# Kernel tuning notes

Measured on AMD Instinct MI355X. Metric: run time of the kernel, lower is better.

## Reference

```python
import math
import jax, jax.numpy as jnp
import numpy as np

B, S, H = 4, 2048, 1024

def setup_inputs() -> dict:
    key = jax.random.key(0)
    k1, k2, k3, k4 = jax.random.split(key, 4)
    X = jax.random.normal(k1, (B, S, H), dtype=jnp.float32)
    attention_mask = jax.random.randint(k2, (B, S), 0, 2).astype(jnp.bool_)
    W = jax.random.normal(k3, (H, 3 * H), dtype=jnp.float32) * (1.0 / math.sqrt(H))
    b = jax.random.normal(k4, (3 * H,), dtype=jnp.float32) * 0.02
    return {"X": X, "attention_mask": attention_mask, "W": W, "b": b}

def reference(X, attention_mask, W, b):
    hidden_dim = X.shape[-1]
    # fused QKV projection: (B,S,3H)
    QKV = X @ W + b
    Q, K, V = jnp.split(QKV, 3, axis=-1)
    # scores: (B, S, S)
    scores = jnp.einsum('bqd,bkd->bqk', Q, K) / math.sqrt(hidden_dim)
    # 2D key-padding mask (B,S) -> broadcast over query dim; True = masked
    mask = attention_mask[:, None, :]  # (B,1,S) broadcasts to (B,S,S)
    scores = jnp.where(mask, -jnp.inf, scores)
    attn = jax.nn.softmax(scores, axis=-1)
    # dropout_rate = 0.0 (eval): identity
    return jnp.einsum('bqk,bkd->bqd', attn, V)
```

## Files before the change

kernel.cpp:

```cpp
#include <hip/hip_runtime.h>
#include <hip/hip_bf16.h>
#include <stdint.h>


typedef __attribute__((ext_vector_type(8))) short bf16x8;
typedef __attribute__((ext_vector_type(4))) float f32x4;

__device__ __forceinline__ void async_cp16(const void* g, void* l) {
  __builtin_amdgcn_global_load_lds(
      (const __attribute__((address_space(1))) void*)g,
      (__attribute__((address_space(3))) void*)l, 16, 0, 0);
}

__global__ void cvt_f32_bf16(const float* __restrict__ s,
                             __hip_bfloat16* __restrict__ d, int n) {
  int i = (blockIdx.x * blockDim.x + threadIdx.x) * 4;
  if (i >= n) return;
  float4 f = *(const float4*)(s + i);
  __hip_bfloat16 o[4];
  o[0] = __float2bfloat16(f.x);
  o[1] = __float2bfloat16(f.y);
  o[2] = __float2bfloat16(f.z);
  o[3] = __float2bfloat16(f.w);
  *(ushort4*)(d + i) = *(const ushort4*)o;
}

__global__ void transpose_cvt_f32(const float* __restrict__ src, int srcld,
                                  __hip_bfloat16* __restrict__ dst, int dstld) {
  __shared__ float tile[32][33];
  int bx = blockIdx.x * 32;
  int by = blockIdx.y * 32;
  int tx = threadIdx.x, ty = threadIdx.y;
#pragma unroll
  for (int j = 0; j < 4; ++j)
    tile[ty + j * 8][tx] = src[(int64_t)(by + ty + j * 8) * srcld + bx + tx];
  __syncthreads();
#pragma unroll
  for (int j = 0; j < 4; ++j)
    dst[(int64_t)(bx + ty + j * 8) * dstld + by + tx] =
        __float2bfloat16(tile[tx][ty + j * 8]);
}

__global__ __launch_bounds__(256) void mask_scan(const int* __restrict__ mask,
                                                 int* __restrict__ idx,
                                                 int* __restrict__ cnt,
                                                 int* __restrict__ cnt_pad) {
  const int b = blockIdx.x;
  mask += b * 2048;
  idx += b * 2048;
  const int t = threadIdx.x;
  const int lane = t & 63, wave = t >> 6;

  int keep[8];
  int local = 0;
#pragma unroll
  for (int j = 0; j < 8; ++j) {
    keep[j] = (mask[t * 8 + j] == 0);
    local += keep[j];
  }
  int pre = local;
#pragma unroll
  for (int off = 1; off <= 32; off <<= 1) {
    int n = __shfl_up(pre, off, 64);
    if (lane >= off) pre += n;
  }
  __shared__ int wsum[4];
  if (lane == 63) wsum[wave] = pre;
  __syncthreads();
  int base = 0;
  for (int w = 0; w < wave; ++w) base += wsum[w];
  int excl = base + pre - local;
#pragma unroll
  for (int j = 0; j < 8; ++j)
    if (keep[j]) idx[excl++] = t * 8 + j;
  if (t == 255) {
    int tot = base + pre;
    cnt[b] = tot;
    cnt_pad[b] = (tot + 127) & ~127;
  }
}

__global__ __launch_bounds__(256) void gemm_qkv(
    const __hip_bfloat16* __restrict__ Xb, const __hip_bfloat16* __restrict__ Wt,
    const float* __restrict__ bias, const int* __restrict__ idx,
    const int* __restrict__ cnt, const int* __restrict__ cnt_pad,
    __hip_bfloat16* __restrict__ Q, __hip_bfloat16* __restrict__ Kc,
    __hip_bfloat16* __restrict__ Vt) {
  const int z = blockIdx.z;
  const int f = blockIdx.x;
  const int xcd = f & 7, loc = f >> 3;
  const int m0 = ((loc & 7) * 2 + (xcd >> 2)) * 128;
  const int n_idx = (loc >> 3) * 4 + (xcd & 3);
  const bool isQ = (n_idx < 8);
  if (!isQ && m0 >= cnt_pad[z]) return;
  const int n0 = (isQ ? n_idx : n_idx - 8) * 128;
  const __hip_bfloat16* A = Xb + (int64_t)z * 2048 * 1024;
  const __hip_bfloat16* Bt = Wt + (isQ ? 0 : (int64_t)1024 * 1024);
  const float* bv = bias + (isQ ? 0 : 1024);

  const int tid = threadIdx.x;
  const int wave = tid >> 6, lane = tid & 63;
  const int quad = lane >> 4, tr = lane & 15;
  const int wm = wave & 1, wn = wave >> 1;

  __shared__ __hip_bfloat16 ls[17408];
  __hip_bfloat16* lsA = ls;
  __hip_bfloat16* lsB = ls + 8192;

  const __hip_bfloat16* gsrc[8];
  __hip_bfloat16* ldst[8];
  {
    const int srow = lane >> 3;
    const int kc = (((lane & 7) ^ srow) * 8);
    const int cz = isQ ? 0 : cnt[z];
    const int* idxz = idx + z * 2048;
#pragma unroll
    for (int cc = 0; cc < 8; ++cc) {
      int c = wave * 8 + cc;
      int isA = (c < 16);
      int cr = isA ? c : (c - 16);
      int row = cr * 8 + srow;
      if (isA) {
        int ar = m0 + row;
        if (!isQ) ar = (ar < cz) ? idxz[ar] : 0;
        gsrc[cc] = A + (int64_t)ar * 1024 + kc;
      } else {
        gsrc[cc] = Bt + (int64_t)(n0 + row) * 1024 + kc;
      }
      ldst[cc] = (isA ? lsA : lsB) + cr * 512;
    }
  }

  f32x4 acc[4][4];
#pragma unroll
  for (int mi = 0; mi < 4; ++mi)
#pragma unroll
    for (int ni = 0; ni < 4; ++ni) acc[mi][ni] = (f32x4){0.f, 0.f, 0.f, 0.f};

  const int t7 = tr & 7;

  for (int k0 = 0; k0 < 1024; k0 += 64) {
    __syncthreads();
#pragma unroll
    for (int cc = 0; cc < 8; ++cc) async_cp16(gsrc[cc] + k0, ldst[cc]);
    __syncthreads();

#pragma unroll
    for (int w = 0; w < 2; ++w) {
      const int sl = ((w << 2) | quad) ^ t7;
      bf16x8 af[4], bfv[4];
#pragma unroll
      for (int mi = 0; mi < 4; ++mi)
        af[mi] = *(const bf16x8*)(lsA + (wm * 64 + mi * 16 + tr) * 64 + sl * 8);
#pragma unroll
      for (int ni = 0; ni < 4; ++ni)
        bfv[ni] = *(const bf16x8*)(lsB + (wn * 64 + ni * 16 + tr) * 64 + sl * 8);
#pragma unroll
      for (int mi = 0; mi < 4; ++mi)
#pragma unroll
        for (int ni = 0; ni < 4; ++ni)
          acc[mi][ni] = __builtin_amdgcn_mfma_f32_16x16x32_bf16(
              af[mi], bfv[ni], acc[mi][ni], 0, 0, 0);
    }
  }

  const int rowbase = m0 + wm * 64;
  const int colbase = n0 + wn * 64;
  if (isQ) {
    __hip_bfloat16* C = Q + (int64_t)z * 2048 * 1024;
#pragma unroll
    for (int ni = 0; ni < 4; ++ni) {
      int col = colbase + ni * 16 + tr;
      float bb = bv[col];
#pragma unroll
      for (int mi = 0; mi < 4; ++mi) {
        int row = rowbase + mi * 16 + quad * 4;
#pragma unroll
        for (int r = 0; r < 4; ++r)
          C[(int64_t)(row + r) * 1024 + col] =
              __float2bfloat16(acc[mi][ni][r] + bb);
      }
    }
  } else if (n0 < 1024) {
    __hip_bfloat16* C = Kc + (int64_t)z * 2048 * 1024;
#pragma unroll
    for (int ni = 0; ni < 4; ++ni) {
      int col = colbase + ni * 16 + tr;
      float bb = bv[col];
#pragma unroll
      for (int mi = 0; mi < 4; ++mi) {
        int row = rowbase + mi * 16 + quad * 4;
#pragma unroll
        for (int r = 0; r < 4; ++r)
          C[(int64_t)(row + r) * 1024 + col] =
              __float2bfloat16(acc[mi][ni][r] + bb);
      }
    }
  } else {
    __syncthreads();
#pragma unroll
    for (int ni = 0; ni < 4; ++ni) {
      int cl = wn * 64 + ni * 16 + tr;
      float bb = bv[colbase + ni * 16 + tr];
#pragma unroll
      for (int mi = 0; mi < 4; ++mi) {
        int rl = wm * 64 + mi * 16 + quad * 4;
        __hip_bfloat16 h[4];
#pragma unroll
        for (int r = 0; r < 4; ++r) h[r] = __float2bfloat16(acc[mi][ni][r] + bb);
        *(ushort4*)(ls + cl * 136 + rl) = *(const ushort4*)h;
      }
    }
    __syncthreads();
    __hip_bfloat16* Vz = Vt + (int64_t)z * 1024 * 2048;
    const int d0 = n0 - 1024;
    const int seg = tid & 15;
#pragma unroll
    for (int p = 0; p < 8; ++p) {
      int d = p * 16 + (tid >> 4);
      bf16x8 v = *(const bf16x8*)(ls + d * 136 + seg * 8);
      *(bf16x8*)(Vz + (int64_t)(d0 + d) * 2048 + m0 + seg * 8) = v;
    }
  }
}

__global__ __launch_bounds__(256) void gemm_scores(
    const __hip_bfloat16* __restrict__ Qb, const __hip_bfloat16* __restrict__ Kc,
    __hip_bfloat16* __restrict__ Sc, float* __restrict__ rowsum,
    const int* __restrict__ cnt, const int* __restrict__ cnt_pad,
    float scale2) {
  const int z = blockIdx.z;
  const int f = blockIdx.x;
  const int xcd = f & 7, loc = f >> 3;
  const int m0 = ((loc & 7) * 2 + (xcd >> 2)) * 128;
  const int n0 = ((loc >> 3) * 4 + (xcd & 3)) * 64;
  if (n0 >= cnt_pad[z]) return;
  const __hip_bfloat16* A = Qb + (int64_t)z * 2048 * 1024;
  const __hip_bfloat16* Bt = Kc + (int64_t)z * 2048 * 1024;

  const int tid = threadIdx.x;
  const int wave = tid >> 6, lane = tid & 63;
  const int quad = lane >> 4, tr = lane & 15;
  const int wm = wave & 1, wn = wave >> 1;

  __shared__ __hip_bfloat16 lsA[128 * 64];
  __shared__ __hip_bfloat16 lsB[64 * 64];

  const __hip_bfloat16* gsrc[6];
  __hip_bfloat16* ldst[6];
  {
    const int srow = lane >> 3;
    const int kc = (((lane & 7) ^ srow) * 8);
#pragma unroll
    for (int cc = 0; cc < 6; ++cc) {
      int c = wave * 6 + cc;
      int isA = (c < 16);
      int cr = isA ? c : (c - 16);
      int row = cr * 8 + srow;
      gsrc[cc] = isA ? (A + (int64_t)(m0 + row) * 1024 + kc)
                     : (Bt + (int64_t)(n0 + row) * 1024 + kc);
      ldst[cc] = (isA ? lsA : lsB) + cr * 512;
    }
  }

  f32x4 acc[4][2];
#pragma unroll
  for (int mi = 0; mi < 4; ++mi)
#pragma unroll
    for (int ni = 0; ni < 2; ++ni) acc[mi][ni] = (f32x4){0.f, 0.f, 0.f, 0.f};

  const int t7 = tr & 7;

  for (int k0 = 0; k0 < 1024; k0 += 64) {
    __syncthreads();
#pragma unroll
    for (int cc = 0; cc < 6; ++cc) async_cp16(gsrc[cc] + k0, ldst[cc]);
    __syncthreads();

#pragma unroll
    for (int w = 0; w < 2; ++w) {
      const int sl = ((w << 2) | quad) ^ t7;
      bf16x8 af[4], bfv[2];
#pragma unroll
      for (int mi = 0; mi < 4; ++mi)
        af[mi] = *(const bf16x8*)(lsA + (wm * 64 + mi * 16 + tr) * 64 + sl * 8);
#pragma unroll
      for (int ni = 0; ni < 2; ++ni)
        bfv[ni] = *(const bf16x8*)(lsB + (wn * 32 + ni * 16 + tr) * 64 + sl * 8);
#pragma unroll
      for (int mi = 0; mi < 4; ++mi)
#pragma unroll
        for (int ni = 0; ni < 2; ++ni)
          acc[mi][ni] = __builtin_amdgcn_mfma_f32_16x16x32_bf16(
              af[mi], bfv[ni], acc[mi][ni], 0, 0, 0);
    }
  }

  const int rowbase = m0 + wm * 64;
  const int colbase = n0 + wn * 32;
  const int cn = cnt[z];
  __hip_bfloat16* C = Sc + (int64_t)z * 2048 * 2048;

  float psum[4][4];
#pragma unroll
  for (int mi = 0; mi < 4; ++mi)
#pragma unroll
    for (int r = 0; r < 4; ++r) psum[mi][r] = 0.f;

#pragma unroll
  for (int ni = 0; ni < 2; ++ni) {
    int col = colbase + ni * 16 + tr;
    bool valid = (col < cn);
#pragma unroll
    for (int mi = 0; mi < 4; ++mi) {
      int row = rowbase + mi * 16 + quad * 4;
#pragma unroll
      for (int r = 0; r < 4; ++r) {
        float e = valid ? exp2f(acc[mi][ni][r] * scale2) : 0.f;
        C[(int64_t)(row + r) * 2048 + col] = __float2bfloat16(e);
        psum[mi][r] += e;
      }
    }
  }
#pragma unroll
  for (int off = 1; off <= 8; off <<= 1)
#pragma unroll
    for (int mi = 0; mi < 4; ++mi)
#pragma unroll
      for (int r = 0; r < 4; ++r)
        psum[mi][r] += __shfl_xor(psum[mi][r], off, 64);
  if (tr == 0) {
    float* rs = rowsum + z * 2048 + rowbase;
#pragma unroll
    for (int mi = 0; mi < 4; ++mi)
#pragma unroll
      for (int r = 0; r < 4; ++r)
        atomicAdd(&rs[mi * 16 + quad * 4 + r], psum[mi][r]);
  }
}

__global__ __launch_bounds__(256) void gemm_pv(
    const __hip_bfloat16* __restrict__ Sc, const __hip_bfloat16* __restrict__ Vt,
    float* __restrict__ out, const float* __restrict__ rowsum,
    const int* __restrict__ cnt_pad) {
  const int z = blockIdx.z;
  const int f = blockIdx.x;
  const int xcd = f & 7, loc = f >> 3;
  const int m0 = ((loc & 7) * 2 + (xcd >> 2)) * 128;
  const int n0 = ((loc >> 3) * 4 + (xcd & 3)) * 64;
  const int Ks = cnt_pad[z];
  const __hip_bfloat16* A = Sc + (int64_t)z * 2048 * 2048;
  const __hip_bfloat16* Bt = Vt + (int64_t)z * 1024 * 2048;

  const int tid = threadIdx.x;
  const int wave = tid >> 6, lane = tid & 63;
  const int quad = lane >> 4, tr = lane & 15;
  const int wm = wave & 1, wn = wave >> 1;

  __shared__ __hip_bfloat16 lsA[128 * 64];
  __shared__ __hip_bfloat16 lsB[64 * 64];

  const __hip_bfloat16* gsrc[6];
  __hip_bfloat16* ldst[6];
  {
    const int srow = lane >> 3;
    const int kc = (((lane & 7) ^ srow) * 8);
#pragma unroll
    for (int cc = 0; cc < 6; ++cc) {
      int c = wave * 6 + cc;
      int isA = (c < 16);
      int cr = isA ? c : (c - 16);
      int row = cr * 8 + srow;
      gsrc[cc] = isA ? (A + (int64_t)(m0 + row) * 2048 + kc)
                     : (Bt + (int64_t)(n0 + row) * 2048 + kc);
      ldst[cc] = (isA ? lsA : lsB) + cr * 512;
    }
  }

  f32x4 acc[4][2];
#pragma unroll
  for (int mi = 0; mi < 4; ++mi)
#pragma unroll
    for (int ni = 0; ni < 2; ++ni) acc[mi][ni] = (f32x4){0.f, 0.f, 0.f, 0.f};

  const int t7 = tr & 7;

  for (int k0 = 0; k0 < Ks; k0 += 64) {
    __syncthreads();
#pragma unroll
    for (int cc = 0; cc < 6; ++cc) async_cp16(gsrc[cc] + k0, ldst[cc]);
    __syncthreads();

#pragma unroll
    for (int w = 0; w < 2; ++w) {
      const int sl = ((w << 2) | quad) ^ t7;
      bf16x8 af[4], bfv[2];
#pragma unroll
      for (int mi = 0; mi < 4; ++mi)
        af[mi] = *(const bf16x8*)(lsA + (wm * 64 + mi * 16 + tr) * 64 + sl * 8);
#pragma unroll
      for (int ni = 0; ni < 2; ++ni)
        bfv[ni] = *(const bf16x8*)(lsB + (wn * 32 + ni * 16 + tr) * 64 + sl * 8);
#pragma unroll
      for (int mi = 0; mi < 4; ++mi)
#pragma unroll
        for (int ni = 0; ni < 2; ++ni)
          acc[mi][ni] = __builtin_amdgcn_mfma_f32_16x16x32_bf16(
              af[mi], bfv[ni], acc[mi][ni], 0, 0, 0);
    }
  }

  const int rowbase = m0 + wm * 64;
  const int colbase = n0 + wn * 32;
  const float* rs = rowsum + z * 2048 + rowbase;
  float invv[4][4];
#pragma unroll
  for (int mi = 0; mi < 4; ++mi)
#pragma unroll
    for (int r = 0; r < 4; ++r) invv[mi][r] = 1.0f / rs[mi * 16 + quad * 4 + r];

  float* C = out + (int64_t)z * 2048 * 1024;
#pragma unroll
  for (int ni = 0; ni < 2; ++ni) {
    int col = colbase + ni * 16 + tr;
#pragma unroll
    for (int mi = 0; mi < 4; ++mi) {
      int row = rowbase + mi * 16 + quad * 4;
#pragma unroll
      for (int r = 0; r < 4; ++r)
        C[(int64_t)(row + r) * 1024 + col] = acc[mi][ni][r] * invv[mi][r];
    }
  }
}

extern "C" void kernel_launch(void* const* d_in, const int* in_sizes, int n_in,
                              void* d_out, int out_size, void* d_ws,
                              size_t ws_size, hipStream_t stream) {
  const float* X = (const float*)d_in[0];
  const int* mask = (const int*)d_in[1];
  const float* W = (const float*)d_in[2];
  const float* bias = (const float*)d_in[3];
  float* out = (float*)d_out;

  char* ws = (char*)d_ws;
  auto alloc = [&](size_t bytes) {
    char* p = ws;
    ws += (bytes + 255) & ~(size_t)255;
    return p;
  };
  __hip_bfloat16* Xb = (__hip_bfloat16*)alloc(8192ULL * 1024 * 2);
  __hip_bfloat16* Wt = (__hip_bfloat16*)alloc(3072ULL * 1024 * 2);
  __hip_bfloat16* Q = (__hip_bfloat16*)alloc(8192ULL * 1024 * 2);
  __hip_bfloat16* Kc = (__hip_bfloat16*)alloc(4ULL * 2048 * 1024 * 2);
  __hip_bfloat16* Vt = (__hip_bfloat16*)alloc(4ULL * 1024 * 2048 * 2);
  __hip_bfloat16* Sc = (__hip_bfloat16*)alloc(4ULL * 2048 * 2048 * 2);
  float* rowsum = (float*)alloc(8192ULL * 4);
  int* idx = (int*)alloc(4ULL * 2048 * 4);
  int* cnt = (int*)alloc(64);
  int* cnt_pad = (int*)alloc(64);

  hipMemsetAsync(rowsum, 0, 8192ULL * 4, stream);
  cvt_f32_bf16<<<8192, 256, 0, stream>>>(X, Xb, 8192 * 1024);
  transpose_cvt_f32<<<dim3(96, 32, 1), dim3(32, 8), 0, stream>>>(W, 3072, Wt,
                                                                 1024);
  mask_scan<<<4, 256, 0, stream>>>(mask, idx, cnt, cnt_pad);
  gemm_qkv<<<dim3(384, 1, 4), 256, 0, stream>>>(Xb, Wt, bias, idx, cnt,
                                                cnt_pad, Q, Kc, Vt);
  gemm_scores<<<dim3(512, 1, 4), 256, 0, stream>>>(
      Q, Kc, Sc, rowsum, cnt, cnt_pad, 0.03125f * 1.4426950408889634f);
  gemm_pv<<<dim3(256, 1, 4), 256, 0, stream>>>(Sc, Vt, out, rowsum, cnt_pad);
}
```

Baseline: 222.7 us.

## Double-buffer LDS tiles in all three GEMMs to overlap loads with MFMA

Converts the single-buffered load-then-compute K loops of the QKV, scores and PV GEMMs into a two-stage ping-pong pipeline. The next tile's async global-to-LDS copies are issued before computing the current tile, with partial vmcnt waits and raw barriers in place of two __syncthreads per iteration. This is meant to hide global memory latency behind the MFMA work. It doubles LDS usage per block, which may reduce occupancy, and the hand-written waitcnt counts must match the number of outstanding copies.

```diff
diff --git a/kernel.cpp b/kernel.cpp
--- a/kernel.cpp
+++ b/kernel.cpp
@@ -11,6 +11,20 @@
       (const __attribute__((address_space(1))) void*)g,
       (__attribute__((address_space(3))) void*)l, 16, 0, 0);
 }
+
+#define PIPE_BARRIER(N)                                     \
+  do {                                                      \
+    asm volatile("s_waitcnt vmcnt(" #N ")" ::: "memory");   \
+    __builtin_amdgcn_s_barrier();                           \
+    asm volatile("" ::: "memory");                          \
+  } while (0)
+
+#define POST_BARRIER()                                      \
+  do {                                                      \
+    asm volatile("s_waitcnt lgkmcnt(0)" ::: "memory");      \
+    __builtin_amdgcn_s_barrier();                           \
+    asm volatile("" ::: "memory");                          \
+  } while (0)
 
 __global__ void cvt_f32_bf16(const float* __restrict__ s,
                              __hip_bfloat16* __restrict__ d, int n) {
@@ -103,12 +117,10 @@
   const int quad = lane >> 4, tr = lane & 15;
   const int wm = wave & 1, wn = wave >> 1;
 
-  __shared__ __hip_bfloat16 ls[17408];
-  __hip_bfloat16* lsA = ls;
-  __hip_bfloat16* lsB = ls + 8192;
+  __shared__ __hip_bfloat16 ls[32768];
 
   const __hip_bfloat16* gsrc[8];
-  __hip_bfloat16* ldst[8];
+  int loff[8];
   {
     const int srow = lane >> 3;
     const int kc = (((lane & 7) ^ srow) * 8);
@@ -127,7 +139,7 @@
       } else {
         gsrc[cc] = Bt + (int64_t)(n0 + row) * 1024 + kc;
       }
-      ldst[cc] = (isA ? lsA : lsB) + cr * 512;
+      loff[cc] = (isA ? 0 : 8192) + cr * 512;
     }
   }
 
@@ -139,30 +151,40 @@
 
   const int t7 = tr & 7;
 
-  for (int k0 = 0; k0 < 1024; k0 += 64) {
-    __syncthreads();
-#pragma unroll
-    for (int cc = 0; cc < 8; ++cc) async_cp16(gsrc[cc] + k0, ldst[cc]);
-    __syncthreads();
-
-#pragma unroll
-    for (int w = 0; w < 2; ++w) {
-      const int sl = ((w << 2) | quad) ^ t7;
-      bf16x8 af[4], bfv[4];
-#pragma unroll
-      for (int mi = 0; mi < 4; ++mi)
-        af[mi] = *(const bf16x8*)(lsA + (wm * 64 + mi * 16 + tr) * 64 + sl * 8);
-#pragma unroll
-      for (int ni = 0; ni < 4; ++ni)
-        bfv[ni] = *(const bf16x8*)(lsB + (wn * 64 + ni * 16 + tr) * 64 + sl * 8);
-#pragma unroll
-      for (int mi = 0; mi < 4; ++mi)
-#pragma unroll
-        for (int ni = 0; ni < 4; ++ni)
-          acc[mi][ni] = __builtin_amdgcn_mfma_f32_16x16x32_bf16(
-              af[mi], bfv[ni], acc[mi][ni], 0, 0, 0);
-    }
-  }
+#define QKV_STAGE(buf, k0)                                        \
+  do {                                                            \
+    _Pragma("unroll") for (int cc = 0; cc < 8; ++cc)              \
+        async_cp16(gsrc[cc] + (k0), ls + (buf)*16384 + loff[cc]); \
+  } while (0)
+
+#define QKV_COMPUTE(buf)                                                       \
+  do {                                                                         \
+    const __hip_bfloat16* lsAc = ls + (buf)*16384;                             \
+    const __hip_bfloat16* lsBc = lsAc + 8192;                                  \
+    _Pragma("unroll") for (int w = 0; w < 2; ++w) {                            \
+      const int sl = ((w << 2) | quad) ^ t7;                                   \
+      bf16x8 af[4], bfv[4];                                                    \
+      _Pragma("unroll") for (int mi = 0; mi < 4; ++mi) af[mi] =                \
+          *(const bf16x8*)(lsAc + (wm * 64 + mi * 16 + tr) * 64 + sl * 8);     \
+      _Pragma("unroll") for (int ni = 0; ni < 4; ++ni) bfv[ni] =               \
+          *(const bf16x8*)(lsBc + (wn * 64 + ni * 16 + tr) * 64 + sl * 8);     \
+      _Pragma("unroll") for (int mi = 0; mi < 4; ++mi)                         \
+          _Pragma("unroll") for (int ni = 0; ni < 4; ++ni) acc[mi][ni] =       \
+              __builtin_amdgcn_mfma_f32_16x16x32_bf16(af[mi], bfv[ni],         \
+                                                      acc[mi][ni], 0, 0, 0);   \
+    }                                                                          \
+  } while (0)
+
+  QKV_STAGE(0, 0);
+  for (int kt = 0; kt < 15; ++kt) {
+    const int cur = kt & 1;
+    QKV_STAGE(cur ^ 1, (kt + 1) * 64);
+    PIPE_BARRIER(8);
+    QKV_COMPUTE(cur);
+    POST_BARRIER();
+  }
+  PIPE_BARRIER(0);
+  QKV_COMPUTE(1);
 
   const int rowbase = m0 + wm * 64;
   const int colbase = n0 + wn * 64;
@@ -222,6 +244,8 @@
       *(bf16x8*)(Vz + (int64_t)(d0 + d) * 2048 + m0 + seg * 8) = v;
     }
   }
+#undef QKV_STAGE
+#undef QKV_COMPUTE
 }
 
 __global__ __launch_bounds__(256) void gemm_scores(
@@ -243,11 +267,10 @@
   const int quad = lane >> 4, tr = lane & 15;
   const int wm = wave & 1, wn = wave >> 1;
 
-  __shared__ __hip_bfloat16 lsA[128 * 64];
-  __shared__ __hip_bfloat16 lsB[64 * 64];
+  __shared__ __hip_bfloat16 ls[24576];
 
   const __hip_bfloat16* gsrc[6];
-  __hip_bfloat16* ldst[6];
+  int loff[6];
   {
     const int srow = lane >> 3;
     const int kc = (((lane & 7) ^ srow) * 8);
@@ -259,7 +282,7 @@
       int row = cr * 8 + srow;
       gsrc[cc] = isA ? (A + (int64_t)(m0 + row) * 1024 + kc)
                      : (Bt + (int64_t)(n0 + row) * 1024 + kc);
-      ldst[cc] = (isA ? lsA : lsB) + cr * 512;
+      loff[cc] = (isA ? 0 : 8192) + cr * 512;
     }
   }
 
@@ -271,30 +294,42 @@
 
   const int t7 = tr & 7;
 
-  for (int k0 = 0; k0 < 1024; k0 += 64) {
-    __syncthreads();
-#pragma unroll
-    for (int cc = 0; cc < 6; ++cc) async_cp16(gsrc[cc] + k0, ldst[cc]);
-    __syncthreads();
-
-#pragma unroll
-    for (int w = 0; w < 2; ++w) {
-      const int sl = ((w << 2) | quad) ^ t7;
-      bf16x8 af[4], bfv[2];
-#pragma unroll
-      for (int mi = 0; mi < 4; ++mi)
-        af[mi] = *(const bf16x8*)(lsA + (wm * 64 + mi * 16 + tr) * 64 + sl * 8);
-#pragma unroll
-      for (int ni = 0; ni < 2; ++ni)
-        bfv[ni] = *(const bf16x8*)(lsB + (wn * 32 + ni * 16 + tr) * 64 + sl * 8);
-#pragma unroll
-      for (int mi = 0; mi < 4; ++mi)
-#pragma unroll
-        for (int ni = 0; ni < 2; ++ni)
-          acc[mi][ni] = __builtin_amdgcn_mfma_f32_16x16x32_bf16(
-              af[mi], bfv[ni], acc[mi][ni], 0, 0, 0);
-    }
-  }
+#define SC_STAGE(buf, k0)                                         \
+  do {                                                            \
+    _Pragma("unroll") for (int cc = 0; cc < 6; ++cc)              \
+        async_cp16(gsrc[cc] + (k0), ls + (buf)*12288 + loff[cc]); \
+  } while (0)
+
+#define SC_COMPUTE(buf)                                                        \
+  do {                                                                         \
+    const __hip_bfloat16* lsAc = ls + (buf)*12288;                             \
+    const __hip_bfloat16* lsBc = lsAc + 8192;                                  \
+    _Pragma("unroll") for (int w = 0; w < 2; ++w) {                            \
+      const int sl = ((w << 2) | quad) ^ t7;                                   \
+      bf16x8 af[4], bfv[2];                                                    \
+      _Pragma("unroll") for (int mi = 0; mi < 4; ++mi) af[mi] =                \
+          *(const bf16x8*)(lsAc + (wm * 64 + mi * 16 + tr) * 64 + sl * 8);     \
+      _Pragma("unroll") for (int ni = 0; ni < 2; ++ni) bfv[ni] =               \
+          *(const bf16x8*)(lsBc + (wn * 32 + ni * 16 + tr) * 64 + sl * 8);     \
+      _Pragma("unroll") for (int mi = 0; mi < 4; ++mi)                         \
+          _Pragma("unroll") for (int ni = 0; ni < 2; ++ni) acc[mi][ni] =       \
+              __builtin_amdgcn_mfma_f32_16x16x32_bf16(af[mi], bfv[ni],         \
+                                                      acc[mi][ni], 0, 0, 0);   \
+    }                                                                          \
+  } while (0)
+
+  SC_STAGE(0, 0);
+  for (int kt = 0; kt < 15; ++kt) {
+    const int cur = kt & 1;
+    SC_STAGE(cur ^ 1, (kt + 1) * 64);
+    PIPE_BARRIER(6);
+    SC_COMPUTE(cur);
+    POST_BARRIER();
+  }
+  PIPE_BARRIER(0);
+  SC_COMPUTE(1);
+#undef SC_STAGE
+#undef SC_COMPUTE
 
   const int rowbase = m0 + wm * 64;
   const int colbase = n0 + wn * 32;
@@ -357,11 +392,10 @@
   const int quad = lane >> 4, tr = lane & 15;
   const int wm = wave & 1, wn = wave >> 1;
 
-  __shared__ __hip_bfloat16 lsA[128 * 64];
-  __shared__ __hip_bfloat16 lsB[64 * 64];
+  __shared__ __hip_bfloat16 ls[24576];
 
   const __hip_bfloat16* gsrc[6];
-  __hip_bfloat16* ldst[6];
+  int loff[6];
   {
     const int srow = lane >> 3;
     const int kc = (((lane & 7) ^ srow) * 8);
@@ -373,7 +407,7 @@
       int row = cr * 8 + srow;
       gsrc[cc] = isA ? (A + (int64_t)(m0 + row) * 2048 + kc)
                      : (Bt + (int64_t)(n0 + row) * 2048 + kc);
-      ldst[cc] = (isA ? lsA : lsB) + cr * 512;
+      loff[cc] = (isA ? 0 : 8192) + cr * 512;
     }
   }
 
@@ -385,30 +419,45 @@
 
   const int t7 = tr & 7;
 
-  for (int k0 = 0; k0 < Ks; k0 += 64) {
-    __syncthreads();
-#pragma unroll
-    for (int cc = 0; cc < 6; ++cc) async_cp16(gsrc[cc] + k0, ldst[cc]);
-    __syncthreads();
-
-#pragma unroll
-    for (int w = 0; w < 2; ++w) {
-      const int sl = ((w << 2) | quad) ^ t7;
-      bf16x8 af[4], bfv[2];
-#pragma unroll
-      for (int mi = 0; mi < 4; ++mi)
-        af[mi] = *(const bf16x8*)(lsA + (wm * 64 + mi * 16 + tr) * 64 + sl * 8);
-#pragma unroll
-      for (int ni = 0; ni < 2; ++ni)
-        bfv[ni] = *(const bf16x8*)(lsB + (wn * 32 + ni * 16 + tr) * 64 + sl * 8);
-#pragma unroll
-      for (int mi = 0; mi < 4; ++mi)
-#pragma unroll
-        for (int ni = 0; ni < 2; ++ni)
-          acc[mi][ni] = __builtin_amdgcn_mfma_f32_16x16x32_bf16(
-              af[mi], bfv[ni], acc[mi][ni], 0, 0, 0);
-    }
-  }
+#define PV_STAGE(buf, k0)                                         \
+  do {                                                            \
+    _Pragma("unroll") for (int cc = 0; cc < 6; ++cc)              \
+        async_cp16(gsrc[cc] + (k0), ls + (buf)*12288 + loff[cc]); \
+  } while (0)
+
+#define PV_COMPUTE(buf)                                                        \
+  do {                                                                         \
+    const __hip_bfloat16* lsAc = ls + (buf)*12288;                             \
+    const __hip_bfloat16* lsBc = lsAc + 8192;                                  \
+    _Pragma("unroll") for (int w = 0; w < 2; ++w) {                            \
+      const int sl = ((w << 2) | quad) ^ t7;                                   \
+      bf16x8 af[4], bfv[2];                                                    \
+      _Pragma("unroll") for (int mi = 0; mi < 4; ++mi) af[mi] =                \
+          *(const bf16x8*)(lsAc + (wm * 64 + mi * 16 + tr) * 64 + sl * 8);     \
+      _Pragma("unroll") for (int ni = 0; ni < 2; ++ni) bfv[ni] =               \
+          *(const bf16x8*)(lsBc + (wn * 32 + ni * 16 + tr) * 64 + sl * 8);     \
+      _Pragma("unroll") for (int mi = 0; mi < 4; ++mi)                         \
+          _Pragma("unroll") for (int ni = 0; ni < 2; ++ni) acc[mi][ni] =       \
+              __builtin_amdgcn_mfma_f32_16x16x32_bf16(af[mi], bfv[ni],         \
+                                                      acc[mi][ni], 0, 0, 0);   \
+    }                                                                          \
+  } while (0)
+
+  const int NT = Ks >> 6;
+  PV_STAGE(0, 0);
+  for (int kt = 0; kt < NT; ++kt) {
+    const int cur = kt & 1;
+    if (kt + 1 < NT) {
+      PV_STAGE(cur ^ 1, (kt + 1) * 64);
+      PIPE_BARRIER(6);
+    } else {
+      PIPE_BARRIER(0);
+    }
+    PV_COMPUTE(cur);
+    POST_BARRIER();
+  }
+#undef PV_STAGE
+#undef PV_COMPUTE
 
   const int rowbase = m0 + wm * 64;
   const int colbase = n0 + wn * 32;
```

New measurement: 213.2 us. 1.04x faster.

## Use 256-row tiles with 8-wave double-buffered ping-pong pipeline in all GEMMs

Applied to the files above, without the earlier changes.

Rewrites the QKV, scores and PV GEMMs to use 512-thread blocks with 256x256 or 256x128 output tiles and a double-buffered LDS pipeline. Async global-to-LDS loads for the next k-slices are interleaved with MFMA phases, using explicit barriers, vmcnt waits and setprio. Padding of the key count is raised to multiples of 256 to match the larger tiles. The aim is to hide load latency and raise data reuse per block, at the cost of more registers and LDS per block, fewer blocks, and extra padded work on masked keys.

```diff
diff --git a/kernel.cpp b/kernel.cpp
--- a/kernel.cpp
+++ b/kernel.cpp
@@ -11,6 +11,15 @@
       (const __attribute__((address_space(1))) void*)g,
       (__attribute__((address_space(3))) void*)l, 16, 0, 0);
 }
+
+#define FENCE() asm volatile("" ::: "memory")
+#define BAR()                           \
+  do {                                  \
+    FENCE();                            \
+    __builtin_amdgcn_s_barrier();       \
+    FENCE();                            \
+  } while (0)
+#define VMW(N) asm volatile("s_waitcnt vmcnt(" #N ")" ::: "memory")
 
 __global__ void cvt_f32_bf16(const float* __restrict__ s,
                              __hip_bfloat16* __restrict__ d, int n) {
@@ -76,11 +85,12 @@
   if (t == 255) {
     int tot = base + pre;
     cnt[b] = tot;
-    cnt_pad[b] = (tot + 127) & ~127;
-  }
-}
-
-__global__ __launch_bounds__(256) void gemm_qkv(
+    int p = (tot + 255) & ~255;
+    cnt_pad[b] = p > 2048 ? 2048 : p;
+  }
+}
+
+__global__ __launch_bounds__(512, 2) void gemm_qkv(
     const __hip_bfloat16* __restrict__ Xb, const __hip_bfloat16* __restrict__ Wt,
     const float* __restrict__ bias, const int* __restrict__ idx,
     const int* __restrict__ cnt, const int* __restrict__ cnt_pad,
@@ -88,83 +98,124 @@
     __hip_bfloat16* __restrict__ Vt) {
   const int z = blockIdx.z;
   const int f = blockIdx.x;
-  const int xcd = f & 7, loc = f >> 3;
-  const int m0 = ((loc & 7) * 2 + (xcd >> 2)) * 128;
-  const int n_idx = (loc >> 3) * 4 + (xcd & 3);
-  const bool isQ = (n_idx < 8);
+  int m0, n0;
+  bool isQ;
+  if (f < 32) {
+    int xcd = f & 7, loc = f >> 3;
+    isQ = true;
+    m0 = (loc * 2 + (xcd >> 2)) * 256;
+    n0 = (xcd & 3) * 256;
+  } else {
+    int g = f - 32, xcd = g & 7, loc = g >> 3;
+    isQ = false;
+    m0 = ((loc & 3) * 2 + (xcd >> 2)) * 256;
+    n0 = ((loc >> 2) * 4 + (xcd & 3)) * 256;
+  }
   if (!isQ && m0 >= cnt_pad[z]) return;
-  const int n0 = (isQ ? n_idx : n_idx - 8) * 128;
   const __hip_bfloat16* A = Xb + (int64_t)z * 2048 * 1024;
   const __hip_bfloat16* Bt = Wt + (isQ ? 0 : (int64_t)1024 * 1024);
   const float* bv = bias + (isQ ? 0 : 1024);
 
   const int tid = threadIdx.x;
   const int wave = tid >> 6, lane = tid & 63;
-  const int quad = lane >> 4, tr = lane & 15;
-  const int wm = wave & 1, wn = wave >> 1;
-
-  __shared__ __hip_bfloat16 ls[17408];
-  __hip_bfloat16* lsA = ls;
-  __hip_bfloat16* lsB = ls + 8192;
-
-  const __hip_bfloat16* gsrc[8];
-  __hip_bfloat16* ldst[8];
+  const int quad = lane >> 4, tr = lane & 15, t7 = tr & 7;
+  const int wm = wave >> 2, wn = wave & 3;
+
+  __shared__ __hip_bfloat16 ls[65536];
+
+  const int srow = lane >> 3;
+  const int kcs = ((lane & 7) ^ srow) * 8;
+
+  const __hip_bfloat16* pA[2][2];
+  const __hip_bfloat16* pB[2][2];
+  int aoff[2][2], boff[2][2];
   {
-    const int srow = lane >> 3;
-    const int kc = (((lane & 7) ^ srow) * 8);
     const int cz = isQ ? 0 : cnt[z];
     const int* idxz = idx + z * 2048;
 #pragma unroll
-    for (int cc = 0; cc < 8; ++cc) {
-      int c = wave * 8 + cc;
-      int isA = (c < 16);
-      int cr = isA ? c : (c - 16);
-      int row = cr * 8 + srow;
-      if (isA) {
-        int ar = m0 + row;
+    for (int h = 0; h < 2; ++h)
+#pragma unroll
+      for (int j = 0; j < 2; ++j) {
+        int chunk = wave * 2 + j;
+        int rl = h * 128 + chunk * 8 + srow;
+        int ar = m0 + rl;
         if (!isQ) ar = (ar < cz) ? idxz[ar] : 0;
-        gsrc[cc] = A + (int64_t)ar * 1024 + kc;
-      } else {
-        gsrc[cc] = Bt + (int64_t)(n0 + row) * 1024 + kc;
-      }
-      ldst[cc] = (isA ? lsA : lsB) + cr * 512;
-    }
-  }
-
-  f32x4 acc[4][4];
-#pragma unroll
-  for (int mi = 0; mi < 4; ++mi)
+        pA[h][j] = A + (int64_t)ar * 1024 + kcs;
+        pB[h][j] = Bt + (int64_t)(n0 + rl) * 1024 + kcs;
+        aoff[h][j] = (h * 128 + chunk * 8) * 64;
+        boff[h][j] = 32768 + (h * 128 + chunk * 8) * 64;
+      }
+  }
+
+  f32x4 acc[8][4];
+#pragma unroll
+  for (int mi = 0; mi < 8; ++mi)
 #pragma unroll
     for (int ni = 0; ni < 4; ++ni) acc[mi][ni] = (f32x4){0.f, 0.f, 0.f, 0.f};
 
-  const int t7 = tr & 7;
-
-  for (int k0 = 0; k0 < 1024; k0 += 64) {
-    __syncthreads();
-#pragma unroll
-    for (int cc = 0; cc < 8; ++cc) async_cp16(gsrc[cc] + k0, ldst[cc]);
-    __syncthreads();
-
-#pragma unroll
-    for (int w = 0; w < 2; ++w) {
-      const int sl = ((w << 2) | quad) ^ t7;
-      bf16x8 af[4], bfv[4];
-#pragma unroll
-      for (int mi = 0; mi < 4; ++mi)
-        af[mi] = *(const bf16x8*)(lsA + (wm * 64 + mi * 16 + tr) * 64 + sl * 8);
-#pragma unroll
-      for (int ni = 0; ni < 4; ++ni)
-        bfv[ni] = *(const bf16x8*)(lsB + (wn * 64 + ni * 16 + tr) * 64 + sl * 8);
-#pragma unroll
-      for (int mi = 0; mi < 4; ++mi)
-#pragma unroll
-        for (int ni = 0; ni < 4; ++ni)
-          acc[mi][ni] = __builtin_amdgcn_mfma_f32_16x16x32_bf16(
-              af[mi], bfv[ni], acc[mi][ni], 0, 0, 0);
-    }
-  }
-
-  const int rowbase = m0 + wm * 64;
+  bf16x8 af[4], bf[4];
+
+#define STA(buf, h, t)                                              \
+  do {                                                              \
+    async_cp16(pA[h][0] + (t) * 64, ls + (buf)*16384 + aoff[h][0]); \
+    async_cp16(pA[h][1] + (t) * 64, ls + (buf)*16384 + aoff[h][1]); \
+  } while (0)
+#define STB(buf, h, t)                                              \
+  do {                                                              \
+    async_cp16(pB[h][0] + (t) * 64, ls + (buf)*16384 + boff[h][0]); \
+    async_cp16(pB[h][1] + (t) * 64, ls + (buf)*16384 + boff[h][1]); \
+  } while (0)
+#define DSA(buf, h, s)                                                        \
+  do {                                                                        \
+    const __hip_bfloat16* LA = ls + (buf)*16384;                              \
+    _Pragma("unroll") for (int j = 0; j < 4; ++j) af[j] =                     \
+        *(const bf16x8*)(LA + (wm * 128 + (h)*64 + j * 16 + tr) * 64 +        \
+                         ((((s) << 2) | quad) ^ t7) * 8);                     \
+  } while (0)
+#define DSB(buf, s)                                                           \
+  do {                                                                        \
+    const __hip_bfloat16* LB = ls + 32768 + (buf)*16384;                      \
+    _Pragma("unroll") for (int n = 0; n < 4; ++n) bf[n] =                     \
+        *(const bf16x8*)(LB + (wn * 64 + n * 16 + tr) * 64 +                  \
+                         ((((s) << 2) | quad) ^ t7) * 8);                     \
+  } while (0)
+#define MF(h)                                                                 \
+  do {                                                                        \
+    __builtin_amdgcn_s_setprio(1);                                            \
+    _Pragma("unroll") for (int j = 0; j < 4; ++j)                             \
+        _Pragma("unroll") for (int n = 0; n < 4; ++n) acc[(h)*4 + j][n] =     \
+            __builtin_amdgcn_mfma_f32_16x16x32_bf16(af[j], bf[n],             \
+                                                    acc[(h)*4 + j][n], 0, 0,  \
+                                                    0);                       \
+    __builtin_amdgcn_s_setprio(0);                                            \
+  } while (0)
+
+  STA(0, 0, 0); STA(0, 1, 0); STB(0, 0, 0); STB(0, 1, 0);
+  STB(1, 0, 1);
+  VMW(2);
+  BAR();
+
+  for (int it = 0; it < 8; ++it) {
+    const int t1 = 2 * it + 1;
+    const int tn0 = (2 * it + 2 < 16) ? 2 * it + 2 : 15;
+    const int tn1 = (2 * it + 3 < 16) ? 2 * it + 3 : 15;
+    DSA(0, 0, 0); DSB(0, 0); STB(1, 1, t1); BAR(); MF(0); BAR();
+    DSA(0, 1, 0);            STA(1, 0, t1); BAR(); MF(1); BAR();
+    DSA(0, 0, 1); DSB(0, 1); STA(1, 1, t1); BAR(); MF(0); BAR();
+    DSA(0, 1, 1);            STB(0, 0, tn0); VMW(2); BAR(); MF(1); BAR();
+    DSA(1, 0, 0); DSB(1, 0); STB(0, 1, tn0); BAR(); MF(0); BAR();
+    DSA(1, 1, 0);            STA(0, 0, tn0); BAR(); MF(1); BAR();
+    DSA(1, 0, 1); DSB(1, 1); STA(0, 1, tn0); BAR(); MF(0); BAR();
+    DSA(1, 1, 1);            STB(1, 0, tn1); VMW(2); BAR(); MF(1); BAR();
+  }
+  asm volatile("s_waitcnt vmcnt(0)" ::: "memory");
+#undef STA
+#undef STB
+#undef DSA
+#undef DSB
+#undef MF
+
+  const int rowbase = m0 + wm * 128;
   const int colbase = n0 + wn * 64;
   if (isQ) {
     __hip_bfloat16* C = Q + (int64_t)z * 2048 * 1024;
@@ -173,7 +224,7 @@
       int col = colbase + ni * 16 + tr;
       float bb = bv[col];
 #pragma unroll
-      for (int mi = 0; mi < 4; ++mi) {
+      for (int mi = 0; mi < 8; ++mi) {
         int row = rowbase + mi * 16 + quad * 4;
 #pragma unroll
         for (int r = 0; r < 4; ++r)
@@ -188,7 +239,7 @@
       int col = colbase + ni * 16 + tr;
       float bb = bv[col];
 #pragma unroll
-      for (int mi = 0; mi < 4; ++mi) {
+      for (int mi = 0; mi < 8; ++mi) {
         int row = rowbase + mi * 16 + quad * 4;
 #pragma unroll
         for (int r = 0; r < 4; ++r)
@@ -197,34 +248,42 @@
       }
     }
   } else {
-    __syncthreads();
-#pragma unroll
-    for (int ni = 0; ni < 4; ++ni) {
-      int cl = wn * 64 + ni * 16 + tr;
-      float bb = bv[colbase + ni * 16 + tr];
-#pragma unroll
-      for (int mi = 0; mi < 4; ++mi) {
-        int rl = wm * 64 + mi * 16 + quad * 4;
-        __hip_bfloat16 h[4];
-#pragma unroll
-        for (int r = 0; r < 4; ++r) h[r] = __float2bfloat16(acc[mi][ni][r] + bb);
-        *(ushort4*)(ls + cl * 136 + rl) = *(const ushort4*)h;
-      }
-    }
-    __syncthreads();
     __hip_bfloat16* Vz = Vt + (int64_t)z * 1024 * 2048;
     const int d0 = n0 - 1024;
-    const int seg = tid & 15;
-#pragma unroll
-    for (int p = 0; p < 8; ++p) {
-      int d = p * 16 + (tid >> 4);
-      bf16x8 v = *(const bf16x8*)(ls + d * 136 + seg * 8);
-      *(bf16x8*)(Vz + (int64_t)(d0 + d) * 2048 + m0 + seg * 8) = v;
+#pragma unroll
+    for (int p = 0; p < 2; ++p) {
+      __syncthreads();
+      if ((wn >> 1) == p) {
+#pragma unroll
+        for (int ni = 0; ni < 4; ++ni) {
+          int cl = (wn & 1) * 64 + ni * 16 + tr;
+          float bb = bv[colbase + ni * 16 + tr];
+#pragma unroll
+          for (int mi = 0; mi < 8; ++mi) {
+            int rl = wm * 128 + mi * 16 + quad * 4;
+            __hip_bfloat16 h4[4];
+#pragma unroll
+            for (int r = 0; r < 4; ++r)
+              h4[r] = __float2bfloat16(acc[mi][ni][r] + bb);
+            *(ushort4*)(ls + cl * 264 + rl) = *(const ushort4*)h4;
+          }
+        }
+      }
+      __syncthreads();
+      const int dloc = tid >> 2;
+      const int sg0 = tid & 3;
+#pragma unroll
+      for (int i = 0; i < 8; ++i) {
+        int seg = i * 4 + sg0;
+        bf16x8 v = *(const bf16x8*)(ls + dloc * 264 + seg * 8);
+        *(bf16x8*)(Vz + (int64_t)(d0 + p * 128 + dloc) * 2048 + m0 + seg * 8) =
+            v;
+      }
     }
   }
 }
 
-__global__ __launch_bounds__(256) void gemm_scores(
+__global__ __launch_bounds__(512, 2) void gemm_scores(
     const __hip_bfloat16* __restrict__ Qb, const __hip_bfloat16* __restrict__ Kc,
     __hip_bfloat16* __restrict__ Sc, float* __restrict__ rowsum,
     const int* __restrict__ cnt, const int* __restrict__ cnt_pad,
@@ -232,78 +291,114 @@
   const int z = blockIdx.z;
   const int f = blockIdx.x;
   const int xcd = f & 7, loc = f >> 3;
-  const int m0 = ((loc & 7) * 2 + (xcd >> 2)) * 128;
-  const int n0 = ((loc >> 3) * 4 + (xcd & 3)) * 64;
+  const int m0 = (loc & 7) * 256;
+  const int n0 = ((loc >> 3) * 8 + xcd) * 128;
   if (n0 >= cnt_pad[z]) return;
   const __hip_bfloat16* A = Qb + (int64_t)z * 2048 * 1024;
   const __hip_bfloat16* Bt = Kc + (int64_t)z * 2048 * 1024;
 
   const int tid = threadIdx.x;
   const int wave = tid >> 6, lane = tid & 63;
-  const int quad = lane >> 4, tr = lane & 15;
-  const int wm = wave & 1, wn = wave >> 1;
-
-  __shared__ __hip_bfloat16 lsA[128 * 64];
-  __shared__ __hip_bfloat16 lsB[64 * 64];
-
-  const __hip_bfloat16* gsrc[6];
-  __hip_bfloat16* ldst[6];
+  const int quad = lane >> 4, tr = lane & 15, t7 = tr & 15 & 7;
+  const int wm = wave >> 2, wn = wave & 3;
+
+  __shared__ __hip_bfloat16 ls[49152];
+
+  const int srow = lane >> 3;
+  const int kcs = ((lane & 7) ^ srow) * 8;
+
+  const __hip_bfloat16* pA[2][2];
+  const __hip_bfloat16* pB[2];
+  int aoff[2][2], boff[2];
   {
-    const int srow = lane >> 3;
-    const int kc = (((lane & 7) ^ srow) * 8);
-#pragma unroll
-    for (int cc = 0; cc < 6; ++cc) {
-      int c = wave * 6 + cc;
-      int isA = (c < 16);
-      int cr = isA ? c : (c - 16);
-      int row = cr * 8 + srow;
-      gsrc[cc] = isA ? (A + (int64_t)(m0 + row) * 1024 + kc)
-                     : (Bt + (int64_t)(n0 + row) * 1024 + kc);
-      ldst[cc] = (isA ? lsA : lsB) + cr * 512;
+#pragma unroll
+    for (int h = 0; h < 2; ++h) {
+#pragma unroll
+      for (int j = 0; j < 2; ++j) {
+        int chunk = wave * 2 + j;
+        int rl = h * 128 + chunk * 8 + srow;
+        pA[h][j] = A + (int64_t)(m0 + rl) * 1024 + kcs;
+        aoff[h][j] = (h * 128 + chunk * 8) * 64;
+      }
+      int rlb = h * 64 + wave * 8 + srow;
+      pB[h] = Bt + (int64_t)(n0 + rlb) * 1024 + kcs;
+      boff[h] = 32768 + (h * 64 + wave * 8) * 64;
     }
   }
 
-  f32x4 acc[4][2];
-#pragma unroll
-  for (int mi = 0; mi < 4; ++mi)
+  f32x4 acc[8][2];
+#pragma unroll
+  for (int mi = 0; mi < 8; ++mi)
 #pragma unroll
     for (int ni = 0; ni < 2; ++ni) acc[mi][ni] = (f32x4){0.f, 0.f, 0.f, 0.f};
 
-  const int t7 = tr & 7;
-
-  for (int k0 = 0; k0 < 1024; k0 += 64) {
-    __syncthreads();
-#pragma unroll
-    for (int cc = 0; cc < 6; ++cc) async_cp16(gsrc[cc] + k0, ldst[cc]);
-    __syncthreads();
-
-#pragma unroll
-    for (int w = 0; w < 2; ++w) {
-      const int sl = ((w << 2) | quad) ^ t7;
-      bf16x8 af[4], bfv[2];
-#pragma unroll
-      for (int mi = 0; mi < 4; ++mi)
-        af[mi] = *(const bf16x8*)(lsA + (wm * 64 + mi * 16 + tr) * 64 + sl * 8);
-#pragma unroll
-      for (int ni = 0; ni < 2; ++ni)
-        bfv[ni] = *(const bf16x8*)(lsB + (wn * 32 + ni * 16 + tr) * 64 + sl * 8);
-#pragma unroll
-      for (int mi = 0; mi < 4; ++mi)
-#pragma unroll
-        for (int ni = 0; ni < 2; ++ni)
-          acc[mi][ni] = __builtin_amdgcn_mfma_f32_16x16x32_bf16(
-              af[mi], bfv[ni], acc[mi][ni], 0, 0, 0);
-    }
-  }
-
-  const int rowbase = m0 + wm * 64;
+  bf16x8 af[4], bf[2];
+
+#define STA(buf, h, t)                                              \
+  do {                                                              \
+    async_cp16(pA[h][0] + (t) * 64, ls + (buf)*16384 + aoff[h][0]); \
+    async_cp16(pA[h][1] + (t) * 64, ls + (buf)*16384 + aoff[h][1]); \
+  } while (0)
+#define STB(buf, h, t) \
+  async_cp16(pB[h] + (t) * 64, ls + (buf)*8192 + boff[h])
+#define DSA(buf, h, s)                                                        \
+  do {                                                                        \
+    const __hip_bfloat16* LA = ls + (buf)*16384;                              \
+    _Pragma("unroll") for (int j = 0; j < 4; ++j) af[j] =                     \
+        *(const bf16x8*)(LA + (wm * 128 + (h)*64 + j * 16 + tr) * 64 +        \
+                         ((((s) << 2) | quad) ^ t7) * 8);                     \
+  } while (0)
+#define DSB(buf, s)                                                           \
+  do {                                                                        \
+    const __hip_bfloat16* LB = ls + 32768 + (buf)*8192;                       \
+    _Pragma("unroll") for (int n = 0; n < 2; ++n) bf[n] =                     \
+        *(const bf16x8*)(LB + (wn * 32 + n * 16 + tr) * 64 +                  \
+                         ((((s) << 2) | quad) ^ t7) * 8);                     \
+  } while (0)
+#define MF(h)                                                                 \
+  do {                                                                        \
+    __builtin_amdgcn_s_setprio(1);                                            \
+    _Pragma("unroll") for (int j = 0; j < 4; ++j)                             \
+        _Pragma("unroll") for (int n = 0; n < 2; ++n) acc[(h)*4 + j][n] =     \
+            __builtin_amdgcn_mfma_f32_16x16x32_bf16(af[j], bf[n],             \
+                                                    acc[(h)*4 + j][n], 0, 0,  \
+                                                    0);                       \
+    __builtin_amdgcn_s_setprio(0);                                            \
+  } while (0)
+
+  STA(0, 0, 0); STA(0, 1, 0); STB(0, 0, 0); STB(0, 1, 0);
+  STB(1, 0, 1);
+  VMW(1);
+  BAR();
+
+  for (int it = 0; it < 8; ++it) {
+    const int t1 = 2 * it + 1;
+    const int tn0 = (2 * it + 2 < 16) ? 2 * it + 2 : 15;
+    const int tn1 = (2 * it + 3 < 16) ? 2 * it + 3 : 15;
+    DSA(0, 0, 0); DSB(0, 0); STB(1, 1, t1); BAR(); MF(0); BAR();
+    DSA(0, 1, 0);            STA(1, 0, t1); BAR(); MF(1); BAR();
+    DSA(0, 0, 1); DSB(0, 1); STA(1, 1, t1); BAR(); MF(0); BAR();
+    DSA(0, 1, 1);            STB(0, 0, tn0); VMW(1); BAR(); MF(1); BAR();
+    DSA(1, 0, 0); DSB(1, 0); STB(0, 1, tn0); BAR(); MF(0); BAR();
+    DSA(1, 1, 0);            STA(0, 0, tn0); BAR(); MF(1); BAR();
+    DSA(1, 0, 1); DSB(1, 1); STA(0, 1, tn0); BAR(); MF(0); BAR();
+    DSA(1, 1, 1);            STB(1, 0, tn1); VMW(1); BAR(); MF(1); BAR();
+  }
+  asm volatile("s_waitcnt vmcnt(0)" ::: "memory");
+#undef STA
+#undef STB
+#undef DSA
+#undef DSB
+#undef MF
+
+  const int rowbase = m0 + wm * 128;
   const int colbase = n0 + wn * 32;
   const int cn = cnt[z];
   __hip_bfloat16* C = Sc + (int64_t)z * 2048 * 2048;
 
-  float psum[4][4];
-#pragma unroll
-  for (int mi = 0; mi < 4; ++mi)
+  float psum[8][4];
+#pragma unroll
+  for (int mi = 0; mi < 8; ++mi)
 #pragma unroll
     for (int r = 0; r < 4; ++r) psum[mi][r] = 0.f;
 
@@ -312,7 +407,7 @@
     int col = colbase + ni * 16 + tr;
     bool valid = (col < cn);
 #pragma unroll
-    for (int mi = 0; mi < 4; ++mi) {
+    for (int mi = 0; mi < 8; ++mi) {
       int row = rowbase + mi * 16 + quad * 4;
 #pragma unroll
       for (int r = 0; r < 4; ++r) {
@@ -325,97 +420,136 @@
 #pragma unroll
   for (int off = 1; off <= 8; off <<= 1)
 #pragma unroll
-    for (int mi = 0; mi < 4; ++mi)
+    for (int mi = 0; mi < 8; ++mi)
 #pragma unroll
       for (int r = 0; r < 4; ++r)
         psum[mi][r] += __shfl_xor(psum[mi][r], off, 64);
   if (tr == 0) {
     float* rs = rowsum + z * 2048 + rowbase;
 #pragma unroll
-    for (int mi = 0; mi < 4; ++mi)
+    for (int mi = 0; mi < 8; ++mi)
 #pragma unroll
       for (int r = 0; r < 4; ++r)
         atomicAdd(&rs[mi * 16 + quad * 4 + r], psum[mi][r]);
   }
 }
 
-__global__ __launch_bounds__(256) void gemm_pv(
+__global__ __launch_bounds__(512, 2) void gemm_pv(
     const __hip_bfloat16* __restrict__ Sc, const __hip_bfloat16* __restrict__ Vt,
     float* __restrict__ out, const float* __restrict__ rowsum,
     const int* __restrict__ cnt_pad) {
   const int z = blockIdx.z;
   const int f = blockIdx.x;
-  const int xcd = f & 7, loc = f >> 3;
-  const int m0 = ((loc & 7) * 2 + (xcd >> 2)) * 128;
-  const int n0 = ((loc >> 3) * 4 + (xcd & 3)) * 64;
+  const int m0 = (f >> 3) * 256;
+  const int n0 = (f & 7) * 128;
   const int Ks = cnt_pad[z];
   const __hip_bfloat16* A = Sc + (int64_t)z * 2048 * 2048;
   const __hip_bfloat16* Bt = Vt + (int64_t)z * 1024 * 2048;
 
   const int tid = threadIdx.x;
   const int wave = tid >> 6, lane = tid & 63;
-  const int quad = lane >> 4, tr = lane & 15;
-  const int wm = wave & 1, wn = wave >> 1;
-
-  __shared__ __hip_bfloat16 lsA[128 * 64];
-  __shared__ __hip_bfloat16 lsB[64 * 64];
-
-  const __hip_bfloat16* gsrc[6];
-  __hip_bfloat16* ldst[6];
+  const int quad = lane >> 4, tr = lane & 15, t7 = tr & 7;
+  const int wm = wave >> 2, wn = wave & 3;
+
+  __shared__ __hip_bfloat16 ls[49152];
+
+  const int srow = lane >> 3;
+  const int kcs = ((lane & 7) ^ srow) * 8;
+
+  const __hip_bfloat16* pA[2][2];
+  const __hip_bfloat16* pB[2];
+  int aoff[2][2], boff[2];
   {
-    const int srow = lane >> 3;
-    const int kc = (((lane & 7) ^ srow) * 8);
-#pragma unroll
-    for (int cc = 0; cc < 6; ++cc) {
-      int c = wave * 6 + cc;
-      int isA = (c < 16);
-      int cr = isA ? c : (c - 16);
-      int row = cr * 8 + srow;
-      gsrc[cc] = isA ? (A + (int64_t)(m0 + row) * 2048 + kc)
-                     : (Bt + (int64_t)(n0 + row) * 2048 + kc);
-      ldst[cc] = (isA ? lsA : lsB) + cr * 512;
+#pragma unroll
+    for (int h = 0; h < 2; ++h) {
+#pragma unroll
+      for (int j = 0; j < 2; ++j) {
+        int chunk = wave * 2 + j;
+        int rl = h * 128 + chunk * 8 + srow;
+        pA[h][j] = A + (int64_t)(m0 + rl) * 2048 + kcs;
+        aoff[h][j] = (h * 128 + chunk * 8) * 64;
+      }
+      int rlb = h * 64 + wave * 8 + srow;
+      pB[h] = Bt + (int64_t)(n0 + rlb) * 2048 + kcs;
+      boff[h] = 32768 + (h * 64 + wave * 8) * 64;
     }
   }
 
-  f32x4 acc[4][2];
-#pragma unroll
-  for (int mi = 0; mi < 4; ++mi)
+  f32x4 acc[8][2];
+#pragma unroll
+  for (int mi = 0; mi < 8; ++mi)
 #pragma unroll
     for (int ni = 0; ni < 2; ++ni) acc[mi][ni] = (f32x4){0.f, 0.f, 0.f, 0.f};
 
-  const int t7 = tr & 7;
-
-  for (int k0 = 0; k0 < Ks; k0 += 64) {
-    __syncthreads();
-#pragma unroll
-    for (int cc = 0; cc < 6; ++cc) async_cp16(gsrc[cc] + k0, ldst[cc]);
-    __syncthreads();
-
-#pragma unroll
-    for (int w = 0; w < 2; ++w) {
-      const int sl = ((w << 2) | quad) ^ t7;
-      bf16x8 af[4], bfv[2];
-#pragma unroll
-      for (int mi = 0; mi < 4; ++mi)
-        af[mi] = *(const bf16x8*)(lsA + (wm * 64 + mi * 16 + tr) * 64 + sl * 8);
-#pragma unroll
-      for (int ni = 0; ni < 2; ++ni)
-        bfv[ni] = *(const bf16x8*)(lsB + (wn * 32 + ni * 16 + tr) * 64 + sl * 8);
-#pragma unroll
-      for (int mi = 0; mi < 4; ++mi)
-#pragma unroll
-        for (int ni = 0; ni < 2; ++ni)
-          acc[mi][ni] = __builtin_amdgcn_mfma_f32_16x16x32_bf16(
-              af[mi], bfv[ni], acc[mi][ni], 0, 0, 0);
-    }
-  }
-
-  const int rowbase = m0 + wm * 64;
+  bf16x8 af[4], bf[2];
+
+#define STA(buf, h, t)                                              \
+  do {                                                              \
+    async_cp16(pA[h][0] + (t) * 64, ls + (buf)*16384 + aoff[h][0]); \
+    async_cp16(pA[h][1] + (t) * 64, ls + (buf)*16384 + aoff[h][1]); \
+  } while (0)
+#define STB(buf, h, t) \
+  async_cp16(pB[h] + (t) * 64, ls + (buf)*8192 + boff[h])
+#define DSA(buf, h, s)                                                        \
+  do {                                                                        \
+    const __hip_bfloat16* LA = ls + (buf)*16384;                              \
+    _Pragma("unroll") for (int j = 0; j < 4; ++j) af[j] =                     \
+        *(const bf16x8*)(LA + (wm * 128 + (h)*64 + j * 16 + tr) * 64 +        \
+                         ((((s) << 2) | quad) ^ t7) * 8);                     \
+  } while (0)
+#define DSB(buf, s)                                                           \
+  do {                                                                        \
+    const __hip_bfloat16* LB = ls + 32768 + (buf)*8192;                       \
+    _Pragma("unroll") for (int n = 0; n < 2; ++n) bf[n] =                     \
+        *(const bf16x8*)(LB + (wn * 32 + n * 16 + tr) * 64 +                  \
+                         ((((s) << 2) | quad) ^ t7) * 8);                     \
+  } while (0)
+#define MF(h)                                                                 \
+  do {                                                                        \
+    __builtin_amdgcn_s_setprio(1);                                            \
+    _Pragma("unroll") for (int j = 0; j < 4; ++j)                             \
+        _Pragma("unroll") for (int n = 0; n < 2; ++n) acc[(h)*4 + j][n] =     \
+            __builtin_amdgcn_mfma_f32_16x16x32_bf16(af[j], bf[n],             \
+                                                    acc[(h)*4 + j][n], 0, 0,  \
+                                                    0);                       \
+    __builtin_amdgcn_s_setprio(0);                                            \
+  } while (0)
+
+  const int NT = Ks >> 6;
+  const int NITER = NT >> 1;
+  const int NTm1 = NT - 1;
+
+  STA(0, 0, 0); STA(0, 1, 0); STB(0, 0, 0); STB(0, 1, 0);
+  STB(1, 0, 1);
+  VMW(1);
+  BAR();
+
+  for (int it = 0; it < NITER; ++it) {
+    const int t1 = 2 * it + 1;
+    const int tn0 = (2 * it + 2 > NTm1) ? NTm1 : 2 * it + 2;
+    const int tn1 = (2 * it + 3 > NTm1) ? NTm1 : 2 * it + 3;
+    DSA(0, 0, 0); DSB(0, 0); STB(1, 1, t1); BAR(); MF(0); BAR();
+    DSA(0, 1, 0);            STA(1, 0, t1); BAR(); MF(1); BAR();
+    DSA(0, 0, 1); DSB(0, 1); STA(1, 1, t1); BAR(); MF(0); BAR();
+    DSA(0, 1, 1);            STB(0, 0, tn0); VMW(1); BAR(); MF(1); BAR();
+    DSA(1, 0, 0); DSB(1, 0); STB(0, 1, tn0); BAR(); MF(0); BAR();
+    DSA(1, 1, 0);            STA(0, 0, tn0); BAR(); MF(1); BAR();
+    DSA(1, 0, 1); DSB(1, 1); STA(0, 1, tn0); BAR(); MF(0); BAR();
+    DSA(1, 1, 1);            STB(1, 0, tn1); VMW(1); BAR(); MF(1); BAR();
+  }
+  asm volatile("s_waitcnt vmcnt(0)" ::: "memory");
+#undef STA
+#undef STB
+#undef DSA
+#undef DSB
+#undef MF
+
+  const int rowbase = m0 + wm * 128;
   const int colbase = n0 + wn * 32;
   const float* rs = rowsum + z * 2048 + rowbase;
-  float invv[4][4];
-#pragma unroll
-  for (int mi = 0; mi < 4; ++mi)
+  float invv[8][4];
+#pragma unroll
+  for (int mi = 0; mi < 8; ++mi)
 #pragma unroll
     for (int r = 0; r < 4; ++r) invv[mi][r] = 1.0f / rs[mi * 16 + quad * 4 + r];
 
@@ -424,7 +558,7 @@
   for (int ni = 0; ni < 2; ++ni) {
     int col = colbase + ni * 16 + tr;
 #pragma unroll
-    for (int mi = 0; mi < 4; ++mi) {
+    for (int mi = 0; mi < 8; ++mi) {
       int row = rowbase + mi * 16 + quad * 4;
 #pragma unroll
       for (int r = 0; r < 4; ++r)
@@ -464,9 +598,9 @@
   transpose_cvt_f32<<<dim3(96, 32, 1), dim3(32, 8), 0, stream>>>(W, 3072, Wt,
                                                                  1024);
   mask_scan<<<4, 256, 0, stream>>>(mask, idx, cnt, cnt_pad);
-  gemm_qkv<<<dim3(384, 1, 4), 256, 0, stream>>>(Xb, Wt, bias, idx, cnt,
-                                                cnt_pad, Q, Kc, Vt);
-  gemm_scores<<<dim3(512, 1, 4), 256, 0, stream>>>(
+  gemm_qkv<<<dim3(96, 1, 4), 512, 0, stream>>>(Xb, Wt, bias, idx, cnt,
+                                               cnt_pad, Q, Kc, Vt);
+  gemm_scores<<<dim3(128, 1, 4), 512, 0, stream>>>(
       Q, Kc, Sc, rowsum, cnt, cnt_pad, 0.03125f * 1.4426950408889634f);
-  gemm_pv<<<dim3(256, 1, 4), 256, 0, stream>>>(Sc, Vt, out, rowsum, cnt_pad);
-}
+  gemm_pv<<<dim3(64, 1, 4), 512, 0, stream>>>(Sc, Vt, out, rowsum, cnt_pad);
+}
```

Result: slower. 235.8 us (+5.9%).
